# Optimization experiments

Measured on AMD Instinct MI355X. Metric: run time of the kernel, lower is better.

The kernel has to match this reference:

```python
import jax, jax.numpy as jnp
import numpy as np

B, S, D, H = 4, 2048, 512, 8
HD = D // H


def rotate_half(t):
    half = t.shape[-1] // 2
    return jnp.concatenate([-t[..., half:], t[..., :half]], axis=-1)


def setup_inputs() -> dict:
    key = jax.random.key(0)
    ks = jax.random.split(key, 8)
    x = jax.random.normal(ks[0], (B, S, D), dtype=jnp.float32)
    # realistic rotary tables built from angles
    inv_freq = 1.0 / (10000.0 ** (jnp.arange(0, D // 2, dtype=jnp.float32) / (D // 2)))
    ang = jnp.arange(S, dtype=jnp.float32)[:, None] * inv_freq[None, :]  # [S, D/2]
    ang = jnp.concatenate([ang, ang], axis=-1)  # [S, D]
    cos_emb = jnp.cos(ang)[None]  # [1, S, D]
    sin_emb = jnp.sin(ang)[None]
    mask = jax.random.randint(ks[1], (B, S, S), 0, 2).astype(jnp.bool_)
    scale = 1.0 / np.sqrt(D)
    wq = jax.random.normal(ks[2], (D, D), dtype=jnp.float32) * scale
    wk = jax.random.normal(ks[3], (D, D), dtype=jnp.float32) * scale
    wv = jax.random.normal(ks[4], (D, D), dtype=jnp.float32) * scale
    wo = jax.random.normal(ks[5], (D, D), dtype=jnp.float32) * scale
    return {"x": x, "cos_emb": cos_emb, "sin_emb": sin_emb, "mask": mask,
            "wq": wq, "wk": wk, "wv": wv, "wo": wo}


def reference(x, cos_emb, sin_emb, mask, wq, wk, wv, wo):
    bsz, seqlen, dim = x.shape
    # projections (weights stored as [in, out])
    xq = x @ wq
    xk = x @ wk
    xv = x @ wv
    # RoPE applied over full dim before head split (as in original)
    xq = xq * cos_emb + rotate_half(xq) * sin_emb
    xk = xk * cos_emb + rotate_half(xk) * sin_emb
    # split heads: [B, H, S, HD]
    xq = xq.reshape(bsz, seqlen, H, HD).transpose(0, 2, 1, 3)
    xk = xk.reshape(bsz, seqlen, H, HD).transpose(0, 2, 1, 3)
    xv = xv.reshape(bsz, seqlen, H, HD).transpose(0, 2, 1, 3)
    scores = jnp.einsum('bhqd,bhkd->bhqk', xq, xk) / jnp.sqrt(jnp.float32(HD))
    scores = scores + (~mask)[:, None].astype(scores.dtype) * (-1e9)
    scores = jax.nn.softmax(scores.astype(jnp.float32), axis=-1).astype(xq.dtype)
    scores = scores * mask[:, None].astype(scores.dtype)
    out = jnp.einsum('bhqk,bhkd->bhqd', scores, xv)
    out = out.transpose(0, 2, 1, 3).reshape(bsz, seqlen, dim)
    return out @ wo
```

## Files before the change

kernel.cpp:

```cpp
#include <hip/hip_runtime.h>
#include <hip/hip_bf16.h>

typedef __bf16 bf16x8 __attribute__((ext_vector_type(8)));
typedef float f32x4 __attribute__((ext_vector_type(4)));
typedef short short8 __attribute__((ext_vector_type(8)));

#define MFMA16(a, b, c) __builtin_amdgcn_mfma_f32_16x16x32_bf16((a), (b), (c), 0, 0, 0)

static constexpr int S = 2048;
static constexpr int D = 512;
static constexpr int HD = 64;
static constexpr int KBLK = 64;
#define QSCALE 0.18033688011112042f

typedef __attribute__((address_space(1))) const unsigned int gu32;
typedef __attribute__((address_space(3))) unsigned int lu32;

__device__ __forceinline__ void gll16(const void* g, void* l) {
  __builtin_amdgcn_global_load_lds((gu32*)g, (lu32*)l, 16, 0, 0);
}

__device__ __forceinline__ unsigned short f2b(float f) {
  return __builtin_bit_cast(unsigned short, __float2bfloat16(f));
}
__device__ __forceinline__ float b2f(unsigned short u) {
  return __builtin_bit_cast(float, (unsigned)u << 16);
}

__global__ void prep_kernel(const float* __restrict__ x, unsigned short* __restrict__ xb,
                            const int* __restrict__ m, unsigned long long* __restrict__ bits,
                            const float* __restrict__ wq, const float* __restrict__ wk,
                            const float* __restrict__ wv, const float* __restrict__ wo,
                            unsigned short* __restrict__ wqkvT, unsigned short* __restrict__ woT) {
  __shared__ float t[64][65];
  const int blk = blockIdx.x;
  const int tid = threadIdx.x;
  if (blk < 4096) {
    int idx = blk * 256 + tid;
    float4 v = ((const float4*)x)[idx];
    ushort4 o;
    o.x = f2b(v.x); o.y = f2b(v.y); o.z = f2b(v.z); o.w = f2b(v.w);
    ((ushort4*)xb)[idx] = o;
  } else if (blk < 6144) {
    const int stride = 2048 * 256;
    const int lane0 = (tid & 63) == 0;
    for (int gid = (blk - 4096) * 256 + tid; gid < 4 * 2048 * 2048; gid += stride) {
      unsigned long long w = __ballot(m[gid] != 0);
      if (lane0) bits[gid >> 6] = w;
    }
  } else {
    const int tt = blk - 6144;
    const int z = tt >> 6, r = tt & 63;
    const float* w = (z == 0) ? wq : (z == 1) ? wk : (z == 2) ? wv : wo;
    unsigned short* dst = (z < 3) ? wqkvT + (size_t)z * 512 * 512 : woT;
    const int i0 = (r & 7) * 64, o0 = (r >> 3) * 64;
    for (int it = 0; it < 16; ++it) {
      int idx = it * 256 + tid;
      int ii = idx >> 6, oo = idx & 63;
      t[oo][ii] = w[(size_t)(i0 + ii) * 512 + o0 + oo];
    }
    __syncthreads();
    for (int it = 0; it < 16; ++it) {
      int idx = it * 256 + tid;
      int oo = idx >> 6, ii = idx & 63;
      dst[(size_t)(o0 + oo) * 512 + i0 + ii] = f2b(t[oo][ii]);
    }
  }
}

__global__ __launch_bounds__(256)
void gemm2(const unsigned short* __restrict__ A, const unsigned short* __restrict__ Bt,
           int M, int N, int K, float* __restrict__ Cf,
           unsigned short* __restrict__ qd, unsigned short* __restrict__ kd,
           unsigned short* __restrict__ vtd, int mode) {
  __shared__ alignas(16) unsigned char smem[36864];
  unsigned short (*lds)[2][4096] = (unsigned short (*)[2][4096])smem;
  const int tid = threadIdx.x;
  const int lane = tid & 63, l15 = lane & 15, lg = lane >> 4;
  const int wave = tid >> 6;
  const int m0 = blockIdx.x * 128, n0 = blockIdx.y * 128;
  const int wm = (wave >> 1) * 64, wn = (wave & 1) * 64;
  const int wbase = wave * 512;
  const int grow = tid >> 2, gcol = (tid & 3) * 8;
  f32x4 acc[4][4] = {};
  const int nt = K / 32;

#define GSTAGE(sb, kk)                                                              \
  do {                                                                              \
    gll16(&A[(size_t)(m0 + grow) * K + (kk) + gcol], &lds[sb][0][wbase]);           \
    gll16(&A[(size_t)(m0 + 64 + grow) * K + (kk) + gcol], &lds[sb][0][2048 + wbase]);\
    gll16(&Bt[(size_t)(n0 + grow) * K + (kk) + gcol], &lds[sb][1][wbase]);          \
    gll16(&Bt[(size_t)(n0 + 64 + grow) * K + (kk) + gcol], &lds[sb][1][2048 + wbase]);\
  } while (0)

  GSTAGE(0, 0);
  asm volatile("s_waitcnt vmcnt(0)" ::: "memory");
  __syncthreads();
  for (int t = 0; t < nt; ++t) {
    const int cur = t & 1;
    if (t + 1 < nt) GSTAGE(cur ^ 1, (t + 1) * 32);
    bf16x8 af[4], bfr[4];
#pragma unroll
    for (int i = 0; i < 4; ++i) {
      af[i]  = *(const bf16x8*)&lds[cur][0][(wm + i * 16 + l15) * 32 + lg * 8];
      bfr[i] = *(const bf16x8*)&lds[cur][1][(wn + i * 16 + l15) * 32 + lg * 8];
    }
    __builtin_amdgcn_s_setprio(1);
#pragma unroll
    for (int i = 0; i < 4; ++i)
#pragma unroll
      for (int j = 0; j < 4; ++j)
        acc[i][j] = MFMA16(af[i], bfr[j], acc[i][j]);
    __builtin_amdgcn_s_setprio(0);
    asm volatile("s_waitcnt vmcnt(0)" ::: "memory");
    __syncthreads();
  }
#undef GSTAGE

  if (mode == 0) {
#pragma unroll
    for (int i = 0; i < 4; ++i)
#pragma unroll
      for (int j = 0; j < 4; ++j)
#pragma unroll
        for (int r = 0; r < 4; ++r)
          Cf[(size_t)(m0 + wm + i * 16 + lg * 4 + r) * N + (n0 + wn + j * 16 + l15)] = acc[i][j][r];
  } else {
    const int sel = n0 >> 9;
    const int nb = (n0 & 511) + wn;
    if (sel < 2) {
      unsigned short* dst = (sel == 0) ? qd : kd;
#pragma unroll
      for (int i = 0; i < 4; ++i)
#pragma unroll
        for (int j = 0; j < 4; ++j)
#pragma unroll
          for (int r = 0; r < 4; ++r) {
            const int m = m0 + wm + i * 16 + lg * 4 + r;
            const int nn = nb + j * 16 + l15;
            dst[(((size_t)(m >> 11) * 8 + (nn >> 6)) * 2048 + (m & 2047)) * 64 + (nn & 63)] =
                f2b(acc[i][j][r]);
          }
    } else {
      unsigned short* tb = (unsigned short*)smem + wave * 4608;
#pragma unroll
      for (int i = 0; i < 4; ++i)
#pragma unroll
        for (int j = 0; j < 4; ++j) {
          ushort4 pk;
          pk.x = f2b(acc[i][j][0]); pk.y = f2b(acc[i][j][1]);
          pk.z = f2b(acc[i][j][2]); pk.w = f2b(acc[i][j][3]);
          *(ushort4*)&tb[(j * 16 + l15) * 72 + i * 16 + lg * 4] = pk;
        }
      const int b0 = m0 >> 11;
      const int s0 = (m0 & 2047) + wm;
      const int g = lane >> 3, c = lane & 7;
#pragma unroll
      for (int rr = 0; rr < 8; ++rr) {
        const int row = rr * 8 + g;
        const int nng = nb + row;
        uint4 v = *(const uint4*)&tb[row * 72 + c * 8];
        *(uint4*)&vtd[(((size_t)(b0 * 8) + (nng >> 6)) * 64 + (nng & 63)) * 2048 + s0 + c * 8] = v;
      }
    }
  }
}

__global__ void rope_pair_kernel(const unsigned short* __restrict__ qpre, const unsigned short* __restrict__ kpre,
                                 const float* __restrict__ cose, const float* __restrict__ sine,
                                 unsigned short* __restrict__ qb, unsigned short* __restrict__ kb) {
  const int idx = blockIdx.x * 256 + threadIdx.x;
  const int hd0 = (idx & 7) * 8;
  const int rr = idx >> 3;
  const int b = rr >> 13, h = (rr >> 11) & 3, s = rr & 2047;
  const size_t lo = ((size_t)(b * 8 + h) * 2048 + s) * 64 + hd0;
  const size_t hi = lo + (size_t)4 * 2048 * 64;
  const int d0 = h * 64 + hd0;
  short8 qlo = *(const short8*)&qpre[lo];
  short8 qhi = *(const short8*)&qpre[hi];
  short8 klo = *(const short8*)&kpre[lo];
  short8 khi = *(const short8*)&kpre[hi];
  float4 c0 = *(const float4*)&cose[(size_t)s * 512 + d0];
  float4 c1 = *(const float4*)&cose[(size_t)s * 512 + d0 + 4];
  float4 s0 = *(const float4*)&sine[(size_t)s * 512 + d0];
  float4 s1 = *(const float4*)&sine[(size_t)s * 512 + d0 + 4];
  float cc[8] = {c0.x, c0.y, c0.z, c0.w, c1.x, c1.y, c1.z, c1.w};
  float ss[8] = {s0.x, s0.y, s0.z, s0.w, s1.x, s1.y, s1.z, s1.w};
  short8 qolo, qohi, kolo, kohi;
#pragma unroll
  for (int j = 0; j < 8; ++j) {
    float ql = b2f((unsigned short)qlo[j]), qh = b2f((unsigned short)qhi[j]);
    float kl = b2f((unsigned short)klo[j]), kh = b2f((unsigned short)khi[j]);
    qolo[j] = (short)f2b((ql * cc[j] - qh * ss[j]) * QSCALE);
    qohi[j] = (short)f2b((qh * cc[j] + ql * ss[j]) * QSCALE);
    kolo[j] = (short)f2b(kl * cc[j] - kh * ss[j]);
    kohi[j] = (short)f2b(kh * cc[j] + kl * ss[j]);
  }
  *(short8*)&qb[lo] = qolo;
  *(short8*)&qb[hi] = qohi;
  *(short8*)&kb[lo] = kolo;
  *(short8*)&kb[hi] = kohi;
}

__global__ __launch_bounds__(512)
void flash_kernel(const unsigned short* __restrict__ qb, const unsigned short* __restrict__ kb,
                  const unsigned short* __restrict__ vtb, const unsigned long long* __restrict__ mbits,
                  float* __restrict__ op0, float* __restrict__ op1,
                  float* __restrict__ ls0, float* __restrict__ ls1) {
  __shared__ alignas(16) unsigned short kv[2][2][4096];
  __shared__ alignas(16) f32x4 btab[16];
  const int tid = threadIdx.x;
  const int wave = tid >> 6, lane = tid & 63;
  const int l15 = lane & 15, lg = lane >> 4;
  const int swz = (l15 & 7) << 4;
  const int wgid = blockIdx.x;
  const int slot = wgid >> 3;
  const int bh = (wgid & 7) * 4 + (slot & 3);
  const int rest = slot >> 2;
  const int kh = rest & 1;
  const int q0 = (rest >> 1) * 256 + wave * 16;
  const int b = bh >> 3, h = bh & 7;
  const int kbase = kh * 1024;
  const unsigned short* Q = qb + ((size_t)bh * S + q0) * HD;
  const unsigned short* Kp = kb + (size_t)bh * S * HD;
  const unsigned short* Vt = vtb + (size_t)bh * HD * S;
  const unsigned long long* MrowA = mbits + ((size_t)b * S + q0 + l15) * (S / 64) + kh * 16;
  const unsigned long long* MrowB = MrowA + (size_t)128 * (S / 64);
  float* opart = kh ? op1 : op0;
  float* lsum = kh ? ls1 : ls0;

  const int srow = tid >> 3;
  const int scol = ((tid & 7) ^ (srow & 7)) * 8;
  const int ksrow = ((srow & 15) >> 2) * 8 + ((srow >> 4) & 1) * 4 + (srow & 3) + (srow >> 5) * 32;
  const int wbase = wave * 512;

  if (tid < 16) {
    f32x4 e;
    e[0] = (tid & 1) ? 0.f : -300.f;
    e[1] = (tid & 2) ? 0.f : -300.f;
    e[2] = (tid & 4) ? 0.f : -300.f;
    e[3] = (tid & 8) ? 0.f : -300.f;
    btab[tid] = e;
  }

  bf16x8 qf0a = *(const bf16x8*)&Q[l15 * HD + lg * 8];
  bf16x8 qf1a = *(const bf16x8*)&Q[l15 * HD + 32 + lg * 8];
  bf16x8 qf0b = *(const bf16x8*)&Q[(128 + l15) * HD + lg * 8];
  bf16x8 qf1b = *(const bf16x8*)&Q[(128 + l15) * HD + 32 + lg * 8];
  f32x4 oa[4] = {}, ob[4] = {};
  float lpa = 0.f, lpb = 0.f;
  const int lgs8 = lg * 8;

  unsigned long long wAa = MrowA[0], wAb = MrowB[0];
  gll16(&Kp[(size_t)(kbase + ksrow) * HD + scol], &kv[0][0][wbase]);
  gll16(&Vt[(size_t)srow * S + kbase + scol], &kv[0][1][wbase]);
  asm volatile("s_waitcnt vmcnt(0) lgkmcnt(0)" ::: "memory");
  __syncthreads();

  for (int t = 0; t < 16; ++t) {
    const int cur = t & 1;
    unsigned long long wBa = 0, wBb = 0;
    if (t + 1 < 16) {
      const int kn = kbase + (t + 1) * KBLK;
      gll16(&Kp[(size_t)(kn + ksrow) * HD + scol], &kv[cur ^ 1][0][wbase]);
      gll16(&Vt[(size_t)srow * S + kn + scol], &kv[cur ^ 1][1][wbase]);
      wBa = MrowA[t + 1];
      wBb = MrowB[t + 1];
    }
    const char* kbp = (const char*)&kv[cur][0][0];
    const char* vbp = (const char*)&kv[cur][1][0];

    bf16x8 pf0a, pf1a, pf0b, pf1b;
#pragma unroll
    for (int n = 0; n < 4; ++n) {
      const int cb = (n * 16 + l15) * 128 + ((lg * 16) ^ swz);
      bf16x8 kf0 = *(const bf16x8*)(kbp + cb);
      bf16x8 kf1 = *(const bf16x8*)(kbp + (cb ^ 64));
      f32x4 scA = {}, scB = {};
      __builtin_amdgcn_s_setprio(1);
      scA = MFMA16(kf0, qf0a, scA);
      scA = MFMA16(kf1, qf1a, scA);
      scB = MFMA16(kf0, qf0b, scB);
      scB = MFMA16(kf1, qf1b, scB);
      __builtin_amdgcn_s_setprio(0);
      const int sh = (n == 0) ? 0 : (n == 1) ? 4 : (n == 2) ? 32 : 36;
      const f32x4 ba = btab[(unsigned)(wAa >> (lgs8 + sh)) & 15u];
      const f32x4 bb = btab[(unsigned)(wAb >> (lgs8 + sh)) & 15u];
      f32x4 pa, pb;
#pragma unroll
      for (int r = 0; r < 4; ++r) {
        pa[r] = __builtin_amdgcn_exp2f(scA[r] + ba[r]);
        pb[r] = __builtin_amdgcn_exp2f(scB[r] + bb[r]);
      }
      lpa += (pa[0] + pa[1]) + (pa[2] + pa[3]);
      lpb += (pb[0] + pb[1]) + (pb[2] + pb[3]);
      bf16x8& dsta = (n < 2) ? pf0a : pf1a;
      bf16x8& dstb = (n < 2) ? pf0b : pf1b;
      const int jo = (n & 1) * 4;
#pragma unroll
      for (int j = 0; j < 4; ++j) {
        dsta[jo + j] = (__bf16)pa[j];
        dstb[jo + j] = (__bf16)pb[j];
      }
    }

    __builtin_amdgcn_s_setprio(1);
#pragma unroll
    for (int n = 0; n < 4; ++n) {
      const int cb = (n * 16 + l15) * 128 + ((lg * 16) ^ swz);
      bf16x8 vf0 = *(const bf16x8*)(vbp + cb);
      bf16x8 vf1 = *(const bf16x8*)(vbp + (cb ^ 64));
      oa[n] = MFMA16(pf0a, vf0, oa[n]);
      oa[n] = MFMA16(pf1a, vf1, oa[n]);
      ob[n] = MFMA16(pf0b, vf0, ob[n]);
      ob[n] = MFMA16(pf1b, vf1, ob[n]);
    }
    __builtin_amdgcn_s_setprio(0);

    asm volatile("s_waitcnt vmcnt(0)" ::: "memory");
    __syncthreads();
    wAa = wBa;
    wAb = wBb;
  }

  lpa += __shfl_xor(lpa, 16);
  lpa += __shfl_xor(lpa, 32);
  lpb += __shfl_xor(lpb, 16);
  lpb += __shfl_xor(lpb, 32);
  if (lg == 0) {
    lsum[(size_t)bh * S + q0 + l15] = lpa;
    lsum[(size_t)bh * S + q0 + 128 + l15] = lpb;
  }
#pragma unroll
  for (int r = 0; r < 4; ++r)
#pragma unroll
    for (int n = 0; n < 4; ++n) {
      opart[((size_t)(b * S + q0 + lg * 4 + r)) * D + h * HD + n * 16 + l15] = oa[n][r];
      opart[((size_t)(b * S + q0 + 128 + lg * 4 + r)) * D + h * HD + n * 16 + l15] = ob[n][r];
    }
}

__global__ __launch_bounds__(256)
void gemm_fused(const float* __restrict__ op0, const float* __restrict__ op1,
                const float* __restrict__ ls0, const float* __restrict__ ls1,
                const unsigned short* __restrict__ Bt, float* __restrict__ C) {
  __shared__ alignas(16) unsigned short ldsA[2][2048];
  __shared__ alignas(16) unsigned short ldsB[2][4096];
  __shared__ float invt[512];
  const int tid = threadIdx.x;
  const int lane = tid & 63, l15 = lane & 15, lg = lane >> 4;
  const int wave = tid >> 6;
  const int m0 = blockIdx.x * 64, n0 = blockIdx.y * 128;
  const int wm = (wave >> 1) * 32, wn = (wave & 1) * 64;
  const int wbase = wave * 512;
  const int grow = tid >> 2, gcol = (tid & 3) * 8;
  const size_t abase = (size_t)(m0 + (tid >> 2)) * 512 + (tid & 3) * 8;
  f32x4 acc[2][4] = {};

  for (int e = tid; e < 512; e += 256) {
    const int row = e >> 3, hh = e & 7;
    const int m = m0 + row;
    const size_t li = ((size_t)((m >> 11) * 8 + hh)) * 2048 + (m & 2047);
    const float l = ls0[li] + ls1[li];
    invt[e] = (l > 0.f) ? 1.f / l : 0.f;
  }

#define BSTAGE(sb, kk)                                                               \
  do {                                                                               \
    gll16(&Bt[(size_t)(n0 + grow) * 512 + (kk) + gcol], &ldsB[sb][wbase]);           \
    gll16(&Bt[(size_t)(n0 + 64 + grow) * 512 + (kk) + gcol], &ldsB[sb][2048 + wbase]);\
  } while (0)

  float4 a0, a1, p0, p1;
#define ALOAD(kk)                                          \
  do {                                                     \
    a0 = *(const float4*)&op0[abase + (kk)];               \
    a1 = *(const float4*)&op0[abase + (kk) + 4];           \
    p0 = *(const float4*)&op1[abase + (kk)];               \
    p1 = *(const float4*)&op1[abase + (kk) + 4];           \
  } while (0)

#define AWRITE(sb, kk)                                                       \
  do {                                                                       \
    const float inv = invt[((tid >> 2) << 3) | ((kk) >> 6)];                 \
    short8 pk;                                                               \
    pk[0] = (short)f2b((a0.x + p0.x) * inv);                                 \
    pk[1] = (short)f2b((a0.y + p0.y) * inv);                                 \
    pk[2] = (short)f2b((a0.z + p0.z) * inv);                                 \
    pk[3] = (short)f2b((a0.w + p0.w) * inv);                                 \
    pk[4] = (short)f2b((a1.x + p1.x) * inv);                                 \
    pk[5] = (short)f2b((a1.y + p1.y) * inv);                                 \
    pk[6] = (short)f2b((a1.z + p1.z) * inv);                                 \
    pk[7] = (short)f2b((a1.w + p1.w) * inv);                                 \
    *(short8*)&ldsA[sb][(tid >> 2) * 32 + (tid & 3) * 8] = pk;               \
  } while (0)

  ALOAD(0);
  BSTAGE(0, 0);
  __syncthreads();
  AWRITE(0, 0);
  __syncthreads();

  for (int t = 0; t < 16; ++t) {
    const int cur = t & 1;
    const bool have = (t + 1 < 16);
    if (have) { ALOAD((t + 1) * 32); BSTAGE(cur ^ 1, (t + 1) * 32); }
    bf16x8 af[2], bfr[4];
#pragma unroll
    for (int i = 0; i < 2; ++i)
      af[i] = *(const bf16x8*)&ldsA[cur][(wm + i * 16 + l15) * 32 + lg * 8];
#pragma unroll
    for (int j = 0; j < 4; ++j)
      bfr[j] = *(const bf16x8*)&ldsB[cur][(wn + j * 16 + l15) * 32 + lg * 8];
    __builtin_amdgcn_s_setprio(1);
#pragma unroll
    for (int i = 0; i < 2; ++i)
#pragma unroll
      for (int j = 0; j < 4; ++j)
        acc[i][j] = MFMA16(af[i], bfr[j], acc[i][j]);
    __builtin_amdgcn_s_setprio(0);
    asm volatile("s_waitcnt vmcnt(0)" ::: "memory");
    __syncthreads();
    if (have) AWRITE(cur ^ 1, (t + 1) * 32);
    __syncthreads();
  }
#undef BSTAGE
#undef ALOAD
#undef AWRITE

#pragma unroll
  for (int i = 0; i < 2; ++i)
#pragma unroll
    for (int j = 0; j < 4; ++j)
#pragma unroll
      for (int r = 0; r < 4; ++r)
        C[(size_t)(m0 + wm + i * 16 + lg * 4 + r) * 512 + (n0 + wn + j * 16 + l15)] = acc[i][j][r];
}

extern "C" void kernel_launch(void* const* d_in, const int* in_sizes, int n_in,
                              void* d_out, int out_size, void* d_ws, size_t ws_size,
                              hipStream_t stream) {
  const float* x = (const float*)d_in[0];
  const float* cose = (const float*)d_in[1];
  const float* sine = (const float*)d_in[2];
  const int* mask = (const int*)d_in[3];
  const float* wq = (const float*)d_in[4];
  const float* wk = (const float*)d_in[5];
  const float* wv = (const float*)d_in[6];
  const float* wo = (const float*)d_in[7];
  float* out = (float*)d_out;
  char* ws = (char*)d_ws;

  unsigned short* xb    = (unsigned short*)(ws);
  unsigned short* wqkvT = (unsigned short*)(ws + 8388608);
  unsigned short* woT   = (unsigned short*)(ws + 9961472);
  unsigned short* qpre  = (unsigned short*)(ws + 10485760);
  unsigned short* kpre  = (unsigned short*)(ws + 18874368);
  unsigned short* qbh   = (unsigned short*)(ws + 35651584);
  unsigned short* kbh   = (unsigned short*)(ws + 44040192);
  unsigned short* vtb   = (unsigned short*)(ws + 52428800);
  unsigned long long* mbits = (unsigned long long*)(ws + 60817408);
  float* op0 = (float*)(ws + 10485760);
  float* op1 = (float*)(ws + 62914560);
  float* ls0 = (float*)(ws + 79691776);
  float* ls1 = (float*)(ws + 79953920);

  prep_kernel<<<6400, 256, 0, stream>>>(x, xb, mask, mbits, wq, wk, wv, wo, wqkvT, woT);
  gemm2<<<dim3(64, 12), 256, 0, stream>>>(xb, wqkvT, 8192, 1536, 512, nullptr, qpre, kpre, vtb, 1);
  rope_pair_kernel<<<1024, 256, 0, stream>>>(qpre, kpre, cose, sine, qbh, kbh);
  flash_kernel<<<512, 512, 0, stream>>>(qbh, kbh, vtb, mbits, op0, op1, ls0, ls1);
  gemm_fused<<<dim3(128, 4), 256, 0, stream>>>(op0, op1, ls0, ls1, woT, out);
}
```

Before: 115.9 us.

## Triple-buffer K/V tiles in flash kernel with two-ahead prefetch

Expands the LDS K/V staging buffer from two to three stages and prefetches the tile two iterations ahead. Partial vmcnt waits replace the full drain, and a raw s_barrier replaces __syncthreads. The aim is to hide more global-load latency behind the MFMA work. It costs extra LDS, which may reduce occupancy, and the vmcnt counts must match the outstanding loads, including the mask-word loads, to stay correct.

Measured after the change: 136.9 us. +18.1%, slower.

```diff
diff --git a/kernel.cpp b/kernel.cpp
--- a/kernel.cpp
+++ b/kernel.cpp
@@ -207,7 +207,7 @@
                   const unsigned short* __restrict__ vtb, const unsigned long long* __restrict__ mbits,
                   float* __restrict__ op0, float* __restrict__ op1,
                   float* __restrict__ ls0, float* __restrict__ ls1) {
-  __shared__ alignas(16) unsigned short kv[2][2][4096];
+  __shared__ alignas(16) unsigned short kv[3][2][4096];
   __shared__ alignas(16) f32x4 btab[16];
   const int tid = threadIdx.x;
   const int wave = tid >> 6, lane = tid & 63;
@@ -251,24 +251,31 @@
   float lpa = 0.f, lpb = 0.f;
   const int lgs8 = lg * 8;
 
+#define FSTAGE(sb, kn)                                                     \
+  do {                                                                     \
+    gll16(&Kp[(size_t)((kn) + ksrow) * HD + scol], &kv[sb][0][wbase]);     \
+    gll16(&Vt[(size_t)srow * S + (kn) + scol], &kv[sb][1][wbase]);         \
+  } while (0)
+
   unsigned long long wAa = MrowA[0], wAb = MrowB[0];
-  gll16(&Kp[(size_t)(kbase + ksrow) * HD + scol], &kv[0][0][wbase]);
-  gll16(&Vt[(size_t)srow * S + kbase + scol], &kv[0][1][wbase]);
-  asm volatile("s_waitcnt vmcnt(0) lgkmcnt(0)" ::: "memory");
-  __syncthreads();
-
+  unsigned long long wBa = MrowA[1], wBb = MrowB[1];
+  FSTAGE(0, kbase);
+  FSTAGE(1, kbase + KBLK);
+  asm volatile("s_waitcnt vmcnt(2) lgkmcnt(0)" ::: "memory");
+  __builtin_amdgcn_s_barrier();
+
+  int bi = 0;
   for (int t = 0; t < 16; ++t) {
-    const int cur = t & 1;
-    unsigned long long wBa = 0, wBb = 0;
-    if (t + 1 < 16) {
-      const int kn = kbase + (t + 1) * KBLK;
-      gll16(&Kp[(size_t)(kn + ksrow) * HD + scol], &kv[cur ^ 1][0][wbase]);
-      gll16(&Vt[(size_t)srow * S + kn + scol], &kv[cur ^ 1][1][wbase]);
-      wBa = MrowA[t + 1];
-      wBb = MrowB[t + 1];
-    }
-    const char* kbp = (const char*)&kv[cur][0][0];
-    const char* vbp = (const char*)&kv[cur][1][0];
+    unsigned long long wCa = 0, wCb = 0;
+    const bool pre = (t + 2 < 16);
+    if (pre) {
+      const int bn = (bi == 0) ? 2 : bi - 1;
+      FSTAGE(bn, kbase + (t + 2) * KBLK);
+      wCa = MrowA[t + 2];
+      wCb = MrowB[t + 2];
+    }
+    const char* kbp = (const char*)&kv[bi][0][0];
+    const char* vbp = (const char*)&kv[bi][1][0];
 
     bf16x8 pf0a, pf1a, pf0b, pf1b;
 #pragma unroll
@@ -317,11 +324,14 @@
     }
     __builtin_amdgcn_s_setprio(0);
 
-    asm volatile("s_waitcnt vmcnt(0)" ::: "memory");
-    __syncthreads();
-    wAa = wBa;
-    wAb = wBb;
-  }
+    if (pre) { asm volatile("s_waitcnt vmcnt(4)" ::: "memory"); }
+    else     { asm volatile("s_waitcnt vmcnt(0)" ::: "memory"); }
+    __builtin_amdgcn_s_barrier();
+    wAa = wBa; wAb = wBb;
+    wBa = wCa; wBb = wCb;
+    bi = (bi == 2) ? 0 : bi + 1;
+  }
+#undef FSTAGE
 
   lpa += __shfl_xor(lpa, 16);
   lpa += __shfl_xor(lpa, 32);
```
